# Kernel tuning notes

Hardware: AMD Instinct MI355X
Metric: run time of the kernel (lower is better)

Reference implementation:

```python
import jax, jax.numpy as jnp
import numpy as np

EPS = 1e-5  # torch InstanceNorm1d default


def _instance_norm_lastdim(t):
    # torch InstanceNorm1d applied to (b*h, n, d): normalizes over last axis d
    # per (b, h, n) with biased variance, no affine.
    mu = jnp.mean(t, axis=-1, keepdims=True)
    var = jnp.var(t, axis=-1, keepdims=True)
    return (t - mu) * jax.lax.rsqrt(var + EPS)


def setup_inputs() -> dict:
    key = jax.random.key(0)
    k1, k2, k3, k4 = jax.random.split(key, 4)
    b, n, dim = 4, 8192, 128
    heads, dim_head = 8, 64
    inner = heads * dim_head
    x = jax.random.normal(k1, (b, n, dim), dtype=jnp.float32)
    # nn.Linear(dim, inner*3, bias=False): weight (out, in); we store transposed (in, out)
    w_qkv = jax.random.normal(k2, (dim, inner * 3), dtype=jnp.float32) * (1.0 / np.sqrt(dim))
    w_out = jax.random.normal(k3, (inner, dim), dtype=jnp.float32) * (1.0 / np.sqrt(inner))
    b_out = jax.random.normal(k4, (dim,), dtype=jnp.float32) * 0.01
    return {"x": x, "w_qkv": w_qkv, "w_out": w_out, "b_out": b_out}


def reference(x, w_qkv, w_out, b_out):
    b, n, _ = x.shape
    heads, dim_head = 8, 64
    qkv = x @ w_qkv  # (b, n, 3*inner)
    q, k, v = jnp.split(qkv, 3, axis=-1)

    def to_heads(t):
        return t.reshape(b, n, heads, dim_head).transpose(0, 2, 1, 3)  # b h n d

    q, k, v = to_heads(q), to_heads(k), to_heads(v)
    # galerkin: norm k and v (InstanceNorm over dim_head axis)
    k = _instance_norm_lastdim(k)
    v = _instance_norm_lastdim(v)
    dots = jnp.einsum('bhnd,bhne->bhde', k, v)      # K^T V, small (d x d)
    out = jnp.einsum('bhnd,bhde->bhne', q, dots) * (1.0 / n)
    out = out.transpose(0, 2, 1, 3).reshape(b, n, heads * dim_head)
    return out @ w_out + b_out
```

## Files before the change

### kernel.cpp

```cpp
#include <hip/hip_runtime.h>

#define NN 8192
#define DIM 128

typedef short short8 __attribute__((ext_vector_type(8)));
typedef float f32x4 __attribute__((ext_vector_type(4)));

__device__ __forceinline__ unsigned short f2bf(float f) {
  unsigned int u = __float_as_uint(f);
  u = (u + 0x7FFFu + ((u >> 16) & 1u)) >> 16;
  return (unsigned short)u;
}
__device__ __forceinline__ unsigned int cvtpk(float a, float b) {
  unsigned int r;
  asm("v_cvt_pk_bf16_f32 %0, %1, %2" : "=v"(r) : "v"(a), "v"(b));
  return r;
}

__global__ __launch_bounds__(256) void kv_dots_kernel(const float* __restrict__ x,
                                                      const float* __restrict__ wqkv,
                                                      float* __restrict__ dots) {
  __shared__ __align__(16) unsigned char smem[49152];
  unsigned char* const XB = smem;
  unsigned char* const KT = smem;
  unsigned char* const VT = smem + 8192;
  unsigned char* const WB = smem + 16384;

  const int t = threadIdx.x;
  const int bx = blockIdx.x;
  const int h = bx >> 7;
  const int p = bx & 127;
  const int b = p >> 5;
  const int chunk = p & 31;
  const int row0 = chunk * 256;

  const int wave = t >> 6;
  const int lane = t & 63;
  const int lb = lane & 15;
  const int kg = lane >> 4;
  const unsigned int lxor = (unsigned int)(lb & 7) << 4;

  {
    const int k = t >> 1;
    const int chalf = t & 1;
    const float* wp = wqkv + (size_t)k * 1536 + (chalf ? (1024 + h * 64) : (512 + h * 64));
    const float4* wp4 = (const float4*)wp;
    const int c0 = chalf * 64;
    float4 wv[16];
    float sum = 0.f;
#pragma unroll
    for (int jj = 0; jj < 16; ++jj) {
      wv[jj] = wp4[jj];
      sum += wv[jj].x + wv[jj].y + wv[jj].z + wv[jj].w;
    }
    const float mean = sum * (1.f / 64.f);
#pragma unroll
    for (int jj = 0; jj < 16; ++jj) {
      const int c = c0 + jj * 4;
      const unsigned int cx0 = (unsigned int)((c + 0) & 7) << 4;
      const unsigned int cx1 = (unsigned int)((c + 1) & 7) << 4;
      const unsigned int cx2 = (unsigned int)((c + 2) & 7) << 4;
      const unsigned int cx3 = (unsigned int)((c + 3) & 7) << 4;
      *(unsigned short*)(WB + (c + 0) * 256 + (((unsigned)(2 * k)) ^ cx0)) = f2bf(wv[jj].x - mean);
      *(unsigned short*)(WB + (c + 1) * 256 + (((unsigned)(2 * k)) ^ cx1)) = f2bf(wv[jj].y - mean);
      *(unsigned short*)(WB + (c + 2) * 256 + (((unsigned)(2 * k)) ^ cx2)) = f2bf(wv[jj].z - mean);
      *(unsigned short*)(WB + (c + 3) * 256 + (((unsigned)(2 * k)) ^ cx3)) = f2bf(wv[jj].w - mean);
    }
  }

  f32x4 dacc[4];
#pragma unroll
  for (int nt = 0; nt < 4; ++nt) dacc[nt] = (f32x4)0.f;

  __syncthreads();

  for (int tile = 0; tile < 4; ++tile) {
    const int rowbase = row0 + tile * 64;

    __syncthreads();

    {
      const int r = t >> 2;
      const int cb = (t & 3) * 32;
      const float4* gp4 = (const float4*)(x + (size_t)(b * NN + rowbase + r) * DIM + cb);
      const unsigned int rxor = (unsigned int)(r & 7) << 4;
#pragma unroll
      for (int jj = 0; jj < 4; ++jj) {
        const float4 v0 = gp4[2 * jj];
        const float4 v1 = gp4[2 * jj + 1];
        uint4 u;
        u.x = cvtpk(v0.x, v0.y);
        u.y = cvtpk(v0.z, v0.w);
        u.z = cvtpk(v1.x, v1.y);
        u.w = cvtpk(v1.z, v1.w);
        *(uint4*)(XB + r * 256 + (((unsigned)(2 * cb + 16 * jj)) ^ rxor)) = u;
      }
    }
    __syncthreads();

    f32x4 acc[8];
#pragma unroll
    for (int ct = 0; ct < 8; ++ct) acc[ct] = (f32x4)0.f;

    const int arow = wave * 16 + lb;
#pragma unroll
    for (int ks = 0; ks < 4; ++ks) {
      const unsigned int koff = (unsigned int)(ks * 64 + kg * 16);
      const short8 a = *(const short8*)(XB + arow * 256 + (koff ^ lxor));
#pragma unroll
      for (int ct = 0; ct < 8; ++ct) {
        const short8 bf = *(const short8*)(WB + (ct * 16 + lb) * 256 + (koff ^ lxor));
        acc[ct] = __builtin_amdgcn_mfma_f32_16x16x32_bf16(a, bf, acc[ct], 0, 0, 0);
      }
    }

    float kscale[4];
#pragma unroll
    for (int e = 0; e < 4; ++e) {
      float sk = acc[0][e] * acc[0][e] + acc[1][e] * acc[1][e] +
                 acc[2][e] * acc[2][e] + acc[3][e] * acc[3][e];
      float sv = acc[4][e] * acc[4][e] + acc[5][e] * acc[5][e] +
                 acc[6][e] * acc[6][e] + acc[7][e] * acc[7][e];
      sk += __shfl_xor(sk, 1); sv += __shfl_xor(sv, 1);
      sk += __shfl_xor(sk, 2); sv += __shfl_xor(sv, 2);
      sk += __shfl_xor(sk, 4); sv += __shfl_xor(sv, 4);
      sk += __shfl_xor(sk, 8); sv += __shfl_xor(sv, 8);
      kscale[e] = rsqrtf(sk * (1.f / 64.f) + 1e-5f) * rsqrtf(sv * (1.f / 64.f) + 1e-5f);
    }

    __syncthreads();

    {
      const unsigned int rb2 = (unsigned int)(32 * wave + kg * 8);
#pragma unroll
      for (int ct = 0; ct < 4; ++ct) {
        uint2 w;
        w.x = cvtpk(acc[ct][0] * kscale[0], acc[ct][1] * kscale[1]);
        w.y = cvtpk(acc[ct][2] * kscale[2], acc[ct][3] * kscale[3]);
        *(uint2*)(KT + (ct * 16 + lb) * 128 + (rb2 ^ lxor)) = w;
      }
#pragma unroll
      for (int ct = 4; ct < 8; ++ct) {
        uint2 w;
        w.x = cvtpk(acc[ct][0], acc[ct][1]);
        w.y = cvtpk(acc[ct][2], acc[ct][3]);
        *(uint2*)(VT + ((ct - 4) * 16 + lb) * 128 + (rb2 ^ lxor)) = w;
      }
    }
    __syncthreads();

#pragma unroll
    for (int ks2 = 0; ks2 < 2; ++ks2) {
      const unsigned int koff = (unsigned int)(ks2 * 64 + kg * 16);
      const short8 a = *(const short8*)(KT + (wave * 16 + lb) * 128 + (koff ^ lxor));
#pragma unroll
      for (int nt = 0; nt < 4; ++nt) {
        const short8 bf = *(const short8*)(VT + (nt * 16 + lb) * 128 + (koff ^ lxor));
        dacc[nt] = __builtin_amdgcn_mfma_f32_16x16x32_bf16(a, bf, dacc[nt], 0, 0, 0);
      }
    }
  }

  float* dp = dots + (size_t)(b * 8 + h) * 4096;
#pragma unroll
  for (int nt = 0; nt < 4; ++nt) {
#pragma unroll
    for (int reg = 0; reg < 4; ++reg) {
      const int d = 16 * wave + kg * 4 + reg;
      const int e = nt * 16 + lb;
      atomicAdd(&dp[d * 64 + e], dacc[nt][reg]);
    }
  }
}

__global__ __launch_bounds__(256) void tw_kernel(const float* __restrict__ wqkv,
                                                 const float* __restrict__ wout,
                                                 const float* __restrict__ dots,
                                                 float* __restrict__ part) {
  __shared__ __align__(16) float ds[64 * 66];
  __shared__ __align__(16) float wqT[64 * 36];
  __shared__ __align__(16) float Ts[32 * 66];
  __shared__ __align__(16) float wos[64 * 132];

  const int blk = blockIdx.x;
  const int bh = blk >> 2;
  const int cq = blk & 3;
  const int h = bh & 7;
  const int t = threadIdx.x;

  for (int i = t; i < 4096; i += 256)
    ds[(i >> 6) * 66 + (i & 63)] = dots[(size_t)bh * 4096 + i];

  for (int i = t; i < 2048; i += 256) {
    const int d = i >> 5;
    const int c = i & 31;
    wqT[d * 36 + c] = wqkv[(size_t)(cq * 32 + c) * 1536 + h * 64 + d];
  }

  for (int i = t; i < 2048; i += 256) {
    const int e = i >> 5;
    const int jj = (i & 31) * 4;
    *(float4*)&wos[e * 132 + jj] = *(const float4*)(wout + (size_t)(h * 64 + e) * 128 + jj);
  }
  __syncthreads();

  {
    const int c = t >> 3;
    const int e0 = (t & 7) * 8;
    float acc[8];
#pragma unroll
    for (int q = 0; q < 8; ++q) acc[q] = 0.f;
    for (int d = 0; d < 64; ++d) {
      const float wq = wqT[d * 36 + c];
      const float4 d0 = *(const float4*)&ds[d * 66 + e0];
      const float4 d1 = *(const float4*)&ds[d * 66 + e0 + 4];
      acc[0] += wq * d0.x; acc[1] += wq * d0.y; acc[2] += wq * d0.z; acc[3] += wq * d0.w;
      acc[4] += wq * d1.x; acc[5] += wq * d1.y; acc[6] += wq * d1.z; acc[7] += wq * d1.w;
    }
    *(float4*)&Ts[c * 66 + e0] = make_float4(acc[0], acc[1], acc[2], acc[3]);
    *(float4*)&Ts[c * 66 + e0 + 4] = make_float4(acc[4], acc[5], acc[6], acc[7]);
  }
  __syncthreads();

  {
    const int c = t >> 3;
    const int j0 = (t & 7) * 16;
    float acc[16];
#pragma unroll
    for (int q = 0; q < 16; ++q) acc[q] = 0.f;
    for (int e = 0; e < 64; ++e) {
      const float tv = Ts[c * 66 + e];
#pragma unroll
      for (int q = 0; q < 16; q += 4) {
        const float4 wv = *(const float4*)&wos[e * 132 + j0 + q];
        acc[q + 0] += tv * wv.x;
        acc[q + 1] += tv * wv.y;
        acc[q + 2] += tv * wv.z;
        acc[q + 3] += tv * wv.w;
      }
    }
    float* pp = part + (size_t)bh * 16384 + (size_t)(cq * 32 + c) * 128 + j0;
#pragma unroll
    for (int q = 0; q < 16; q += 4)
      *(float4*)&pp[q] = make_float4(acc[q], acc[q + 1], acc[q + 2], acc[q + 3]);
  }
}

__global__ __launch_bounds__(256) void bigw_reduce(const float* __restrict__ part,
                                                   float* __restrict__ bigw) {
  const int i = blockIdx.x * 256 + threadIdx.x;
  const int b = i >> 14;
  const int cj = i & 16383;
  const float* pp = part + (size_t)b * 8 * 16384 + cj;
  float s = 0.f;
#pragma unroll
  for (int h = 0; h < 8; ++h) s += pp[h * 16384];
  bigw[i] = s * (1.f / (float)NN);
}

__global__ __launch_bounds__(256) void out_kernel(const float* __restrict__ x,
                                                  const float* __restrict__ bigw,
                                                  const float* __restrict__ bout,
                                                  float* __restrict__ out) {
  __shared__ __align__(16) unsigned char smem[49152];
  unsigned char* const XB = smem;
  unsigned char* const WB = smem + 16384;

  const int t = threadIdx.x;
  const int bx = blockIdx.x;
  const int b = bx >> 7;
  const int rowbase = (bx & 127) * 64;

  const int wave = t >> 6;
  const int lane = t & 63;
  const int lb = lane & 15;
  const int kg = lane >> 4;
  const unsigned int lxor = (unsigned int)(lb & 7) << 4;

  {
    const int c = t >> 1;
    const int jhalf = t & 1;
    const float4* wp4 = (const float4*)(bigw + (size_t)b * 16384 + (size_t)c * 128 + jhalf * 64);
    const int j0 = jhalf * 64;
#pragma unroll
    for (int q = 0; q < 16; ++q) {
      const float4 v = wp4[q];
      const int j = j0 + q * 4;
      const unsigned int jx0 = (unsigned int)((j + 0) & 7) << 4;
      const unsigned int jx1 = (unsigned int)((j + 1) & 7) << 4;
      const unsigned int jx2 = (unsigned int)((j + 2) & 7) << 4;
      const unsigned int jx3 = (unsigned int)((j + 3) & 7) << 4;
      *(unsigned short*)(WB + (j + 0) * 256 + (((unsigned)(2 * c)) ^ jx0)) = f2bf(v.x);
      *(unsigned short*)(WB + (j + 1) * 256 + (((unsigned)(2 * c)) ^ jx1)) = f2bf(v.y);
      *(unsigned short*)(WB + (j + 2) * 256 + (((unsigned)(2 * c)) ^ jx2)) = f2bf(v.z);
      *(unsigned short*)(WB + (j + 3) * 256 + (((unsigned)(2 * c)) ^ jx3)) = f2bf(v.w);
    }
  }

  float bias[8];
#pragma unroll
  for (int ct = 0; ct < 8; ++ct) bias[ct] = bout[ct * 16 + lb];

  {
    const int r = t >> 2;
    const int cb = (t & 3) * 32;
    const float4* gp4 = (const float4*)(x + (size_t)(b * NN + rowbase + r) * DIM + cb);
    const unsigned int rxor = (unsigned int)(r & 7) << 4;
#pragma unroll
    for (int jj = 0; jj < 4; ++jj) {
      const float4 v0 = gp4[2 * jj];
      const float4 v1 = gp4[2 * jj + 1];
      uint4 u;
      u.x = cvtpk(v0.x, v0.y);
      u.y = cvtpk(v0.z, v0.w);
      u.z = cvtpk(v1.x, v1.y);
      u.w = cvtpk(v1.z, v1.w);
      *(uint4*)(XB + r * 256 + (((unsigned)(2 * cb + 16 * jj)) ^ rxor)) = u;
    }
  }
  __syncthreads();

  f32x4 acc[8];
#pragma unroll
  for (int ct = 0; ct < 8; ++ct) acc[ct] = (f32x4)0.f;

  const int arow = wave * 16 + lb;
#pragma unroll
  for (int ks = 0; ks < 4; ++ks) {
    const unsigned int koff = (unsigned int)(ks * 64 + kg * 16);
    const short8 a = *(const short8*)(XB + arow * 256 + (koff ^ lxor));
#pragma unroll
    for (int ct = 0; ct < 8; ++ct) {
      const short8 bf = *(const short8*)(WB + (ct * 16 + lb) * 256 + (koff ^ lxor));
      acc[ct] = __builtin_amdgcn_mfma_f32_16x16x32_bf16(a, bf, acc[ct], 0, 0, 0);
    }
  }

  float* op = out + (size_t)(b * NN + rowbase + 16 * wave + kg * 4) * DIM;
#pragma unroll
  for (int ct = 0; ct < 8; ++ct) {
#pragma unroll
    for (int reg = 0; reg < 4; ++reg) {
      op[reg * DIM + ct * 16 + lb] = acc[ct][reg] + bias[ct];
    }
  }
}

extern "C" void kernel_launch(void* const* d_in, const int* in_sizes, int n_in,
                              void* d_out, int out_size, void* d_ws, size_t ws_size,
                              hipStream_t stream) {
  (void)in_sizes; (void)n_in; (void)out_size; (void)ws_size;
  const float* x = (const float*)d_in[0];
  const float* wqkv = (const float*)d_in[1];
  const float* wout = (const float*)d_in[2];
  const float* bout = (const float*)d_in[3];
  float* out = (float*)d_out;

  float* dots = (float*)d_ws;
  float* part = dots + 131072;
  float* bigw = part + 524288;

  hipMemsetAsync(dots, 0, 131072 * sizeof(float), stream);
  hipLaunchKernelGGL(kv_dots_kernel, dim3(1024), dim3(256), 0, stream, x, wqkv, dots);
  hipLaunchKernelGGL(tw_kernel, dim3(128), dim3(256), 0, stream, wqkv, wout, dots, part);
  hipLaunchKernelGGL(bigw_reduce, dim3(256), dim3(256), 0, stream, part, bigw);
  hipLaunchKernelGGL(out_kernel, dim3(512), dim3(256), 0, stream, x, bigw, bout, out);
}
```

Before: 79.01 us.

## Pre-convert x and weights to swizzled bf16 images and stream via global_load_lds

Adds a prep kernel that converts x into a pre-swizzled bf16 tile image and builds mean-centred bf16 weight images once per head. kv_dots and the output GEMM then pull these images straight into LDS with global_load_lds, double-buffering the x tiles in kv_dots. The reduced projection matrix is also emitted as a bf16 swizzled image. This removes the repeated fp32 reads and in-kernel conversion, since x was previously read and converted 8 times in kv_dots (once per head). The cost is an extra kernel launch, an extra pass writing an 8MB image, and a larger workspace requirement, with the old path kept as a fallback.

```diff
diff --git a/kernel.cpp b/kernel.cpp
--- a/kernel.cpp
+++ b/kernel.cpp
@@ -16,10 +16,384 @@
   asm("v_cvt_pk_bf16_f32 %0, %1, %2" : "=v"(r) : "v"(a), "v"(b));
   return r;
 }
-
-__global__ __launch_bounds__(256) void kv_dots_kernel(const float* __restrict__ x,
-                                                      const float* __restrict__ wqkv,
-                                                      float* __restrict__ dots) {
+__device__ __forceinline__ void gll16(const void* gsrc, void* ldst) {
+  __builtin_amdgcn_global_load_lds(
+      (const __attribute__((address_space(1))) unsigned int*)gsrc,
+      (__attribute__((address_space(3))) unsigned int*)ldst, 16, 0, 0);
+}
+#define BAR_LGKM()                                          \
+  do {                                                      \
+    asm volatile("s_waitcnt lgkmcnt(0)" ::: "memory");      \
+    __builtin_amdgcn_sched_barrier(0);                      \
+    __builtin_amdgcn_s_barrier();                           \
+    __builtin_amdgcn_sched_barrier(0);                      \
+  } while (0)
+#define BAR_VM()                                            \
+  do {                                                      \
+    asm volatile("s_waitcnt vmcnt(0)" ::: "memory");        \
+    __builtin_amdgcn_sched_barrier(0);                      \
+    __builtin_amdgcn_s_barrier();                           \
+    __builtin_amdgcn_sched_barrier(0);                      \
+  } while (0)
+
+__global__ __launch_bounds__(256) void prep_kernel(const float* __restrict__ x,
+                                                   const float* __restrict__ wqkv,
+                                                   unsigned char* __restrict__ ximg,
+                                                   unsigned char* __restrict__ wimg) {
+  __shared__ __align__(16) unsigned char wb[32768];
+  const int t = threadIdx.x;
+  const int bx = blockIdx.x;
+  if (bx < 1024) {
+#pragma unroll
+    for (int rep = 0; rep < 2; ++rep) {
+      const int idx = bx * 512 + rep * 256 + t;
+      const int bt = idx >> 10;
+      const int o = (idx & 1023) << 4;
+      const int r = o >> 8;
+      const int q0 = o & 255;
+      const int c0 = (q0 ^ ((r & 7) << 4)) >> 1;
+      const float* src = x + ((size_t)(bt >> 7) * NN + (size_t)(bt & 127) * 64 + r) * DIM + c0;
+      const float4 v0 = *(const float4*)src;
+      const float4 v1 = *(const float4*)(src + 4);
+      uint4 u;
+      u.x = cvtpk(v0.x, v0.y);
+      u.y = cvtpk(v0.z, v0.w);
+      u.z = cvtpk(v1.x, v1.y);
+      u.w = cvtpk(v1.z, v1.w);
+      *(uint4*)(ximg + (size_t)idx * 16) = u;
+    }
+  } else {
+    const int h = bx - 1024;
+    const int k = t >> 1;
+    const int chalf = t & 1;
+    const float* wp = wqkv + (size_t)k * 1536 + (chalf ? (1024 + h * 64) : (512 + h * 64));
+    const float4* wp4 = (const float4*)wp;
+    const int c0 = chalf * 64;
+    float4 wv[16];
+    float sum = 0.f;
+#pragma unroll
+    for (int jj = 0; jj < 16; ++jj) {
+      wv[jj] = wp4[jj];
+      sum += wv[jj].x + wv[jj].y + wv[jj].z + wv[jj].w;
+    }
+    const float mean = sum * (1.f / 64.f);
+#pragma unroll
+    for (int jj = 0; jj < 16; ++jj) {
+      const int c = c0 + jj * 4;
+      const unsigned int cx0 = (unsigned int)((c + 0) & 7) << 4;
+      const unsigned int cx1 = (unsigned int)((c + 1) & 7) << 4;
+      const unsigned int cx2 = (unsigned int)((c + 2) & 7) << 4;
+      const unsigned int cx3 = (unsigned int)((c + 3) & 7) << 4;
+      *(unsigned short*)(wb + (c + 0) * 256 + (((unsigned)(2 * k)) ^ cx0)) = f2bf(wv[jj].x - mean);
+      *(unsigned short*)(wb + (c + 1) * 256 + (((unsigned)(2 * k)) ^ cx1)) = f2bf(wv[jj].y - mean);
+      *(unsigned short*)(wb + (c + 2) * 256 + (((unsigned)(2 * k)) ^ cx2)) = f2bf(wv[jj].z - mean);
+      *(unsigned short*)(wb + (c + 3) * 256 + (((unsigned)(2 * k)) ^ cx3)) = f2bf(wv[jj].w - mean);
+    }
+    __syncthreads();
+    const uint4* s4 = (const uint4*)(wb + t * 128);
+    uint4* d4 = (uint4*)(wimg + (size_t)h * 32768 + t * 128);
+#pragma unroll
+    for (int i = 0; i < 8; ++i) d4[i] = s4[i];
+  }
+}
+
+__global__ __launch_bounds__(256) void kv_dots_v2(const unsigned char* __restrict__ ximg,
+                                                  const unsigned char* __restrict__ wimg,
+                                                  float* __restrict__ dots) {
+  __shared__ __align__(16) unsigned char smem[81920];
+  unsigned char* const XB0 = smem;
+  unsigned char* const XB1 = smem + 16384;
+  unsigned char* const WB = smem + 32768;
+  unsigned char* const KT = smem + 65536;
+  unsigned char* const VT = smem + 73728;
+
+  const int t = threadIdx.x;
+  const int bx = blockIdx.x;
+  const int h = bx >> 7;
+  const int p = bx & 127;
+  const int b = p >> 5;
+  const int chunk = p & 31;
+
+  const int wave = t >> 6;
+  const int lane = t & 63;
+  const int lb = lane & 15;
+  const int kg = lane >> 4;
+  const unsigned int lxor = (unsigned int)(lb & 7) << 4;
+
+  const unsigned char* wsrc = wimg + (size_t)h * 32768;
+  const unsigned char* xsrc = ximg + (size_t)(b * 128 + chunk * 4) * 16384;
+
+#pragma unroll
+  for (int i = 0; i < 8; ++i)
+    gll16(wsrc + (wave * 8 + i) * 1024 + lane * 16, WB + (wave * 8 + i) * 1024);
+#pragma unroll
+  for (int i = 0; i < 4; ++i)
+    gll16(xsrc + (wave * 4 + i) * 1024 + lane * 16, XB0 + (wave * 4 + i) * 1024);
+
+  f32x4 dacc[4];
+#pragma unroll
+  for (int nt = 0; nt < 4; ++nt) dacc[nt] = (f32x4)0.f;
+
+  BAR_VM();
+
+  unsigned char* XBc = XB0;
+  unsigned char* XBn = XB1;
+  const int arow = wave * 16 + lb;
+
+  for (int tile = 0; tile < 4; ++tile) {
+    if (tile < 3) {
+#pragma unroll
+      for (int i = 0; i < 4; ++i)
+        gll16(xsrc + (size_t)(tile + 1) * 16384 + (wave * 4 + i) * 1024 + lane * 16,
+              XBn + (wave * 4 + i) * 1024);
+    }
+
+    f32x4 acc[8];
+#pragma unroll
+    for (int ct = 0; ct < 8; ++ct) acc[ct] = (f32x4)0.f;
+#pragma unroll
+    for (int ks = 0; ks < 4; ++ks) {
+      const unsigned int koff = (unsigned int)(ks * 64 + kg * 16);
+      const short8 a = *(const short8*)(XBc + arow * 256 + (koff ^ lxor));
+#pragma unroll
+      for (int ct = 0; ct < 8; ++ct) {
+        const short8 bf = *(const short8*)(WB + (ct * 16 + lb) * 256 + (koff ^ lxor));
+        acc[ct] = __builtin_amdgcn_mfma_f32_16x16x32_bf16(a, bf, acc[ct], 0, 0, 0);
+      }
+    }
+
+    float kscale[4];
+#pragma unroll
+    for (int e = 0; e < 4; ++e) {
+      float sk = acc[0][e] * acc[0][e] + acc[1][e] * acc[1][e] +
+                 acc[2][e] * acc[2][e] + acc[3][e] * acc[3][e];
+      float sv = acc[4][e] * acc[4][e] + acc[5][e] * acc[5][e] +
+                 acc[6][e] * acc[6][e] + acc[7][e] * acc[7][e];
+      sk += __shfl_xor(sk, 1); sv += __shfl_xor(sv, 1);
+      sk += __shfl_xor(sk, 2); sv += __shfl_xor(sv, 2);
+      sk += __shfl_xor(sk, 4); sv += __shfl_xor(sv, 4);
+      sk += __shfl_xor(sk, 8); sv += __shfl_xor(sv, 8);
+      kscale[e] = rsqrtf(sk * (1.f / 64.f) + 1e-5f) * rsqrtf(sv * (1.f / 64.f) + 1e-5f);
+    }
+
+    {
+      const unsigned int rb2 = (unsigned int)(32 * wave + kg * 8);
+#pragma unroll
+      for (int ct = 0; ct < 4; ++ct) {
+        uint2 w;
+        w.x = cvtpk(acc[ct][0] * kscale[0], acc[ct][1] * kscale[1]);
+        w.y = cvtpk(acc[ct][2] * kscale[2], acc[ct][3] * kscale[3]);
+        *(uint2*)(KT + (ct * 16 + lb) * 128 + (rb2 ^ lxor)) = w;
+      }
+#pragma unroll
+      for (int ct = 4; ct < 8; ++ct) {
+        uint2 w;
+        w.x = cvtpk(acc[ct][0], acc[ct][1]);
+        w.y = cvtpk(acc[ct][2], acc[ct][3]);
+        *(uint2*)(VT + ((ct - 4) * 16 + lb) * 128 + (rb2 ^ lxor)) = w;
+      }
+    }
+    BAR_LGKM();
+
+#pragma unroll
+    for (int ks2 = 0; ks2 < 2; ++ks2) {
+      const unsigned int koff = (unsigned int)(ks2 * 64 + kg * 16);
+      const short8 a = *(const short8*)(KT + (wave * 16 + lb) * 128 + (koff ^ lxor));
+#pragma unroll
+      for (int nt = 0; nt < 4; ++nt) {
+        const short8 bf = *(const short8*)(VT + (nt * 16 + lb) * 128 + (koff ^ lxor));
+        dacc[nt] = __builtin_amdgcn_mfma_f32_16x16x32_bf16(a, bf, dacc[nt], 0, 0, 0);
+      }
+    }
+    BAR_VM();
+
+    unsigned char* tmp = XBc; XBc = XBn; XBn = tmp;
+  }
+
+  float* dp = dots + (size_t)(b * 8 + h) * 4096;
+#pragma unroll
+  for (int nt = 0; nt < 4; ++nt) {
+#pragma unroll
+    for (int reg = 0; reg < 4; ++reg) {
+      const int d = 16 * wave + kg * 4 + reg;
+      const int e = nt * 16 + lb;
+      atomicAdd(&dp[d * 64 + e], dacc[nt][reg]);
+    }
+  }
+}
+
+template <int TR>
+__global__ __launch_bounds__(256) void tw_kernel(const float* __restrict__ wqkv,
+                                                 const float* __restrict__ wout,
+                                                 const float* __restrict__ dots,
+                                                 float* __restrict__ part) {
+  __shared__ __align__(16) float ds[64 * 66];
+  __shared__ __align__(16) float wqT[64 * 36];
+  __shared__ __align__(16) float Ts[32 * 66];
+  __shared__ __align__(16) float wos[64 * 132];
+
+  const int blk = blockIdx.x;
+  const int bh = blk >> 2;
+  const int cq = blk & 3;
+  const int h = bh & 7;
+  const int t = threadIdx.x;
+
+  for (int i = t; i < 4096; i += 256)
+    ds[(i >> 6) * 66 + (i & 63)] = dots[(size_t)bh * 4096 + i];
+
+  for (int i = t; i < 2048; i += 256) {
+    const int d = i >> 5;
+    const int c = i & 31;
+    wqT[d * 36 + c] = wqkv[(size_t)(cq * 32 + c) * 1536 + h * 64 + d];
+  }
+
+  for (int i = t; i < 2048; i += 256) {
+    const int e = i >> 5;
+    const int jj = (i & 31) * 4;
+    *(float4*)&wos[e * 132 + jj] = *(const float4*)(wout + (size_t)(h * 64 + e) * 128 + jj);
+  }
+  __syncthreads();
+
+  {
+    const int c = t >> 3;
+    const int e0 = (t & 7) * 8;
+    float acc[8];
+#pragma unroll
+    for (int q = 0; q < 8; ++q) acc[q] = 0.f;
+    for (int d = 0; d < 64; ++d) {
+      const float wq = wqT[d * 36 + c];
+      const float4 d0 = *(const float4*)&ds[d * 66 + e0];
+      const float4 d1 = *(const float4*)&ds[d * 66 + e0 + 4];
+      acc[0] += wq * d0.x; acc[1] += wq * d0.y; acc[2] += wq * d0.z; acc[3] += wq * d0.w;
+      acc[4] += wq * d1.x; acc[5] += wq * d1.y; acc[6] += wq * d1.z; acc[7] += wq * d1.w;
+    }
+    *(float4*)&Ts[c * 66 + e0] = make_float4(acc[0], acc[1], acc[2], acc[3]);
+    *(float4*)&Ts[c * 66 + e0 + 4] = make_float4(acc[4], acc[5], acc[6], acc[7]);
+  }
+  __syncthreads();
+
+  {
+    const int c = t >> 3;
+    const int j0 = (t & 7) * 16;
+    float acc[16];
+#pragma unroll
+    for (int q = 0; q < 16; ++q) acc[q] = 0.f;
+    for (int e = 0; e < 64; ++e) {
+      const float tv = Ts[c * 66 + e];
+#pragma unroll
+      for (int q = 0; q < 16; q += 4) {
+        const float4 wv = *(const float4*)&wos[e * 132 + j0 + q];
+        acc[q + 0] += tv * wv.x;
+        acc[q + 1] += tv * wv.y;
+        acc[q + 2] += tv * wv.z;
+        acc[q + 3] += tv * wv.w;
+      }
+    }
+    if (TR) {
+      float* pp = part + (size_t)bh * 16384;
+      const int cc = cq * 32 + c;
+#pragma unroll
+      for (int q = 0; q < 16; ++q) pp[(j0 + q) * 128 + cc] = acc[q];
+    } else {
+      float* pp = part + (size_t)bh * 16384 + (size_t)(cq * 32 + c) * 128 + j0;
+#pragma unroll
+      for (int q = 0; q < 16; q += 4)
+        *(float4*)&pp[q] = make_float4(acc[q], acc[q + 1], acc[q + 2], acc[q + 3]);
+    }
+  }
+}
+
+__global__ __launch_bounds__(256) void bigw_reduce_v2(const float* __restrict__ part,
+                                                      unsigned char* __restrict__ bigwimg) {
+  const int idx = blockIdx.x * 256 + threadIdx.x;
+  const int b = idx >> 11;
+  const int o = (idx & 2047) << 4;
+  const int j = o >> 8;
+  const int q0 = o & 255;
+  const int c0 = (q0 ^ ((j & 7) << 4)) >> 1;
+  float s[8];
+#pragma unroll
+  for (int i = 0; i < 8; ++i) s[i] = 0.f;
+  const float* pb = part + (size_t)b * 8 * 16384 + j * 128 + c0;
+#pragma unroll
+  for (int hh = 0; hh < 8; ++hh) {
+    const float4 p0 = *(const float4*)(pb + hh * 16384);
+    const float4 p1 = *(const float4*)(pb + hh * 16384 + 4);
+    s[0] += p0.x; s[1] += p0.y; s[2] += p0.z; s[3] += p0.w;
+    s[4] += p1.x; s[5] += p1.y; s[6] += p1.z; s[7] += p1.w;
+  }
+  const float inv_n = 1.f / (float)NN;
+  uint4 u;
+  u.x = cvtpk(s[0] * inv_n, s[1] * inv_n);
+  u.y = cvtpk(s[2] * inv_n, s[3] * inv_n);
+  u.z = cvtpk(s[4] * inv_n, s[5] * inv_n);
+  u.w = cvtpk(s[6] * inv_n, s[7] * inv_n);
+  *(uint4*)(bigwimg + (size_t)idx * 16) = u;
+}
+
+__global__ __launch_bounds__(256) void out_v2(const unsigned char* __restrict__ ximg,
+                                              const unsigned char* __restrict__ bigwimg,
+                                              const float* __restrict__ bout,
+                                              float* __restrict__ out) {
+  __shared__ __align__(16) unsigned char smem[49152];
+  unsigned char* const XB = smem;
+  unsigned char* const WJ = smem + 16384;
+
+  const int t = threadIdx.x;
+  const int bx = blockIdx.x;
+  const int b = bx >> 7;
+  const int tile = bx & 127;
+
+  const int wave = t >> 6;
+  const int lane = t & 63;
+  const int lb = lane & 15;
+  const int kg = lane >> 4;
+  const unsigned int lxor = (unsigned int)(lb & 7) << 4;
+
+  const unsigned char* wsrc = bigwimg + (size_t)b * 32768;
+  const unsigned char* xsrc = ximg + (size_t)(b * 128 + tile) * 16384;
+
+#pragma unroll
+  for (int i = 0; i < 8; ++i)
+    gll16(wsrc + (wave * 8 + i) * 1024 + lane * 16, WJ + (wave * 8 + i) * 1024);
+#pragma unroll
+  for (int i = 0; i < 4; ++i)
+    gll16(xsrc + (wave * 4 + i) * 1024 + lane * 16, XB + (wave * 4 + i) * 1024);
+
+  float bias[8];
+#pragma unroll
+  for (int ct = 0; ct < 8; ++ct) bias[ct] = bout[ct * 16 + lb];
+
+  BAR_VM();
+
+  f32x4 acc[8];
+#pragma unroll
+  for (int ct = 0; ct < 8; ++ct) acc[ct] = (f32x4)0.f;
+  const int arow = wave * 16 + lb;
+#pragma unroll
+  for (int ks = 0; ks < 4; ++ks) {
+    const unsigned int koff = (unsigned int)(ks * 64 + kg * 16);
+    const short8 a = *(const short8*)(XB + arow * 256 + (koff ^ lxor));
+#pragma unroll
+    for (int ct = 0; ct < 8; ++ct) {
+      const short8 bf = *(const short8*)(WJ + (ct * 16 + lb) * 256 + (koff ^ lxor));
+      acc[ct] = __builtin_amdgcn_mfma_f32_16x16x32_bf16(a, bf, acc[ct], 0, 0, 0);
+    }
+  }
+
+  float* op = out + (size_t)(b * NN + tile * 64 + 16 * wave + kg * 4) * DIM;
+#pragma unroll
+  for (int ct = 0; ct < 8; ++ct) {
+#pragma unroll
+    for (int reg = 0; reg < 4; ++reg) {
+      op[reg * DIM + ct * 16 + lb] = acc[ct][reg] + bias[ct];
+    }
+  }
+}
+
+__global__ __launch_bounds__(256) void kv_dots_fb(const float* __restrict__ x,
+                                                  const float* __restrict__ wqkv,
+                                                  float* __restrict__ dots) {
   __shared__ __align__(16) unsigned char smem[49152];
   unsigned char* const XB = smem;
   unsigned char* const KT = smem;
@@ -76,9 +450,7 @@
 
   for (int tile = 0; tile < 4; ++tile) {
     const int rowbase = row0 + tile * 64;
-
     __syncthreads();
-
     {
       const int r = t >> 2;
       const int cb = (t & 3) * 32;
@@ -101,7 +473,6 @@
     f32x4 acc[8];
 #pragma unroll
     for (int ct = 0; ct < 8; ++ct) acc[ct] = (f32x4)0.f;
-
     const int arow = wave * 16 + lb;
 #pragma unroll
     for (int ks = 0; ks < 4; ++ks) {
@@ -129,7 +500,6 @@
     }
 
     __syncthreads();
-
     {
       const unsigned int rb2 = (unsigned int)(32 * wave + kg * 8);
 #pragma unroll
@@ -173,81 +543,8 @@
   }
 }
 
-__global__ __launch_bounds__(256) void tw_kernel(const float* __restrict__ wqkv,
-                                                 const float* __restrict__ wout,
-                                                 const float* __restrict__ dots,
-                                                 float* __restrict__ part) {
-  __shared__ __align__(16) float ds[64 * 66];
-  __shared__ __align__(16) float wqT[64 * 36];
-  __shared__ __align__(16) float Ts[32 * 66];
-  __shared__ __align__(16) float wos[64 * 132];
-
-  const int blk = blockIdx.x;
-  const int bh = blk >> 2;
-  const int cq = blk & 3;
-  const int h = bh & 7;
-  const int t = threadIdx.x;
-
-  for (int i = t; i < 4096; i += 256)
-    ds[(i >> 6) * 66 + (i & 63)] = dots[(size_t)bh * 4096 + i];
-
-  for (int i = t; i < 2048; i += 256) {
-    const int d = i >> 5;
-    const int c = i & 31;
-    wqT[d * 36 + c] = wqkv[(size_t)(cq * 32 + c) * 1536 + h * 64 + d];
-  }
-
-  for (int i = t; i < 2048; i += 256) {
-    const int e = i >> 5;
-    const int jj = (i & 31) * 4;
-    *(float4*)&wos[e * 132 + jj] = *(const float4*)(wout + (size_t)(h * 64 + e) * 128 + jj);
-  }
-  __syncthreads();
-
-  {
-    const int c = t >> 3;
-    const int e0 = (t & 7) * 8;
-    float acc[8];
-#pragma unroll
-    for (int q = 0; q < 8; ++q) acc[q] = 0.f;
-    for (int d = 0; d < 64; ++d) {
-      const float wq = wqT[d * 36 + c];
-      const float4 d0 = *(const float4*)&ds[d * 66 + e0];
-      const float4 d1 = *(const float4*)&ds[d * 66 + e0 + 4];
-      acc[0] += wq * d0.x; acc[1] += wq * d0.y; acc[2] += wq * d0.z; acc[3] += wq * d0.w;
-      acc[4] += wq * d1.x; acc[5] += wq * d1.y; acc[6] += wq * d1.z; acc[7] += wq * d1.w;
-    }
-    *(float4*)&Ts[c * 66 + e0] = make_float4(acc[0], acc[1], acc[2], acc[3]);
-    *(float4*)&Ts[c * 66 + e0 + 4] = make_float4(acc[4], acc[5], acc[6], acc[7]);
-  }
-  __syncthreads();
-
-  {
-    const int c = t >> 3;
-    const int j0 = (t & 7) * 16;
-    float acc[16];
-#pragma unroll
-    for (int q = 0; q < 16; ++q) acc[q] = 0.f;
-    for (int e = 0; e < 64; ++e) {
-      const float tv = Ts[c * 66 + e];
-#pragma unroll
-      for (int q = 0; q < 16; q += 4) {
-        const float4 wv = *(const float4*)&wos[e * 132 + j0 + q];
-        acc[q + 0] += tv * wv.x;
-        acc[q + 1] += tv * wv.y;
-        acc[q + 2] += tv * wv.z;
-        acc[q + 3] += tv * wv.w;
-      }
-    }
-    float* pp = part + (size_t)bh * 16384 + (size_t)(cq * 32 + c) * 128 + j0;
-#pragma unroll
-    for (int q = 0; q < 16; q += 4)
-      *(float4*)&pp[q] = make_float4(acc[q], acc[q + 1], acc[q + 2], acc[q + 3]);
-  }
-}
-
-__global__ __launch_bounds__(256) void bigw_reduce(const float* __restrict__ part,
-                                                   float* __restrict__ bigw) {
+__global__ __launch_bounds__(256) void bigw_reduce_fb(const float* __restrict__ part,
+                                                      float* __restrict__ bigw) {
   const int i = blockIdx.x * 256 + threadIdx.x;
   const int b = i >> 14;
   const int cj = i & 16383;
@@ -258,10 +555,10 @@
   bigw[i] = s * (1.f / (float)NN);
 }
 
-__global__ __launch_bounds__(256) void out_kernel(const float* __restrict__ x,
-                                                  const float* __restrict__ bigw,
-                                                  const float* __restrict__ bout,
-                                                  float* __restrict__ out) {
+__global__ __launch_bounds__(256) void out_fb(const float* __restrict__ x,
+                                              const float* __restrict__ bigw,
+                                              const float* __restrict__ bout,
+                                              float* __restrict__ out) {
   __shared__ __align__(16) unsigned char smem[49152];
   unsigned char* const XB = smem;
   unsigned char* const WB = smem + 16384;
@@ -323,7 +620,6 @@
   f32x4 acc[8];
 #pragma unroll
   for (int ct = 0; ct < 8; ++ct) acc[ct] = (f32x4)0.f;
-
   const int arow = wave * 16 + lb;
 #pragma unroll
   for (int ks = 0; ks < 4; ++ks) {
@@ -349,20 +645,35 @@
 extern "C" void kernel_launch(void* const* d_in, const int* in_sizes, int n_in,
                               void* d_out, int out_size, void* d_ws, size_t ws_size,
                               hipStream_t stream) {
-  (void)in_sizes; (void)n_in; (void)out_size; (void)ws_size;
+  (void)in_sizes; (void)n_in; (void)out_size;
   const float* x = (const float*)d_in[0];
   const float* wqkv = (const float*)d_in[1];
   const float* wout = (const float*)d_in[2];
   const float* bout = (const float*)d_in[3];
   float* out = (float*)d_out;
 
-  float* dots = (float*)d_ws;
-  float* part = dots + 131072;
-  float* bigw = part + 524288;
-
-  hipMemsetAsync(dots, 0, 131072 * sizeof(float), stream);
-  hipLaunchKernelGGL(kv_dots_kernel, dim3(1024), dim3(256), 0, stream, x, wqkv, dots);
-  hipLaunchKernelGGL(tw_kernel, dim3(128), dim3(256), 0, stream, wqkv, wout, dots, part);
-  hipLaunchKernelGGL(bigw_reduce, dim3(256), dim3(256), 0, stream, part, bigw);
-  hipLaunchKernelGGL(out_kernel, dim3(512), dim3(256), 0, stream, x, bigw, bout, out);
-}
+  const size_t NEED = 8388608ull + 262144ull + 131072ull + 524288ull + 2097152ull;
+  if (ws_size >= NEED) {
+    unsigned char* ximg = (unsigned char*)d_ws;
+    unsigned char* wimg = ximg + 8388608;
+    unsigned char* bigwimg = wimg + 262144;
+    float* dots = (float*)(bigwimg + 131072);
+    float* part = dots + 131072;
+
+    hipMemsetAsync(dots, 0, 131072 * sizeof(float), stream);
+    hipLaunchKernelGGL(prep_kernel, dim3(1032), dim3(256), 0, stream, x, wqkv, ximg, wimg);
+    hipLaunchKernelGGL(kv_dots_v2, dim3(1024), dim3(256), 0, stream, ximg, wimg, dots);
+    hipLaunchKernelGGL((tw_kernel<1>), dim3(128), dim3(256), 0, stream, wqkv, wout, dots, part);
+    hipLaunchKernelGGL(bigw_reduce_v2, dim3(32), dim3(256), 0, stream, part, bigwimg);
+    hipLaunchKernelGGL(out_v2, dim3(512), dim3(256), 0, stream, ximg, bigwimg, bout, out);
+  } else {
+    float* dots = (float*)d_ws;
+    float* part = dots + 131072;
+    float* bigw = part + 524288;
+    hipMemsetAsync(dots, 0, 131072 * sizeof(float), stream);
+    hipLaunchKernelGGL(kv_dots_fb, dim3(1024), dim3(256), 0, stream, x, wqkv, dots);
+    hipLaunchKernelGGL((tw_kernel<0>), dim3(128), dim3(256), 0, stream, wqkv, wout, dots, part);
+    hipLaunchKernelGGL(bigw_reduce_fb, dim3(256), dim3(256), 0, stream, part, bigw);
+    hipLaunchKernelGGL(out_fb, dim3(512), dim3(256), 0, stream, x, bigw, bout, out);
+  }
+}
```

Result: faster. 75.32 us (-4.7%).
